# Kernel tuning notes

Hardware: AMD Instinct MI355X
Metric: run time of the kernel (lower is better)

## Reference

```python
import jax, jax.numpy as jnp
import numpy as np

B, SQ, SK, H, DH = 4, 4096, 462, 10, 64  # batch, img tokens, text tokens, heads, head dim


def setup_inputs() -> dict:
    key = jax.random.key(0)
    k1, k2, k3, k4, k5 = jax.random.split(key, 5)
    q = jax.random.normal(k1, (B, SQ, H * DH), dtype=jnp.float32)
    k = jax.random.normal(k2, (B, SK, H * DH), dtype=jnp.float32)
    v = jax.random.normal(k3, (B, SK, H * DH), dtype=jnp.float32)
    # mask_scale = H*W / sum(mask) in the original -> positive, >= 1
    mask_scale = 1.0 + 3.0 * jax.random.uniform(k4, (B, H, SQ, SK), dtype=jnp.float32)
    mask_bool = jax.random.randint(k5, (B, H, SQ, SK), 0, 2).astype(bool)
    # guarantee every query row attends to at least one key (avoid all -inf rows)
    mask_bool = mask_bool.at[..., 0].set(True)
    return {"q": q, "k": k, "v": v, "mask_bool": mask_bool,
            "mask_scale": mask_scale, "heads": H}


def reference(q, k, v, mask_bool, mask_scale, heads):
    b, sq, d = q.shape
    dh = d // heads
    # [b, s, h*dh] -> [b, h, s, dh]
    qh = q.reshape(b, sq, heads, dh).transpose(0, 2, 1, 3)
    kh = k.reshape(b, -1, heads, dh).transpose(0, 2, 1, 3)
    vh = v.reshape(b, -1, heads, dh).transpose(0, 2, 1, 3)
    scale = 1.0 / np.sqrt(dh).astype(np.float32)
    scores = jnp.einsum("bhqd,bhkd->bhqk", qh, kh) * scale
    scores = scores * mask_scale
    scores = jnp.where(mask_bool, scores, -jnp.inf)
    attn = jax.nn.softmax(scores, axis=-1)
    out = jnp.einsum("bhqk,bhkd->bhqd", attn, vh)
    return out.transpose(0, 2, 1, 3).reshape(b, sq, d)
```

## Files before the change

kernel.cpp:

```cpp
#include <hip/hip_runtime.h>

#define B_  4
#define SQ_ 4096
#define SK_ 462
#define H_  10
#define DH_ 64
#define D_  (H_ * DH_)
#define SKP_ 480
#define KT_  15
#define MBDW_ 16

typedef _Float16 half8 __attribute__((ext_vector_type(8)));
typedef float floatx4 __attribute__((ext_vector_type(4)));
typedef float float2v __attribute__((ext_vector_type(2)));

#define K16_ELEMS ((size_t)B_ * H_ * SKP_ * DH_)
#define MBITS_DW  ((size_t)B_ * H_ * SQ_ * MBDW_)
#define WS_KV     (2 * K16_ELEMS * sizeof(_Float16))
#define WS_FULL   (WS_KV + MBITS_DW * 4)

__device__ int g_mask_fmt;

__global__ void detect_mask_fmt(const unsigned int* __restrict__ mb_dw) {
  __shared__ int s_float, s_byte;
  if (threadIdx.x == 0) { s_float = 0; s_byte = 0; }
  __syncthreads();
  int fl = 0, by = 0;
  for (int i = threadIdx.x; i < 1024; i += 256) {
    unsigned int x = mb_dw[i];
    if (x > 1u) {
      if (x == 0x3F800000u) fl = 1; else by = 1;
    }
  }
  if (fl) atomicOr(&s_float, 1);
  if (by) atomicOr(&s_byte, 1);
  __syncthreads();
  if (threadIdx.x == 0) g_mask_fmt = s_float ? 2 : (s_byte ? 1 : 0);
}

__device__ __forceinline__ half8 cvt8(float4 a, float4 b) {
  half8 o;
  o[0] = (_Float16)a.x; o[1] = (_Float16)a.y;
  o[2] = (_Float16)a.z; o[3] = (_Float16)a.w;
  o[4] = (_Float16)b.x; o[5] = (_Float16)b.y;
  o[6] = (_Float16)b.z; o[7] = (_Float16)b.w;
  return o;
}

__global__ void convert_kv(const float* __restrict__ k, const float* __restrict__ v,
                           _Float16* __restrict__ k16, _Float16* __restrict__ vt16) {
  int t = blockIdx.x * 256 + threadIdx.x;
  const int NK = B_ * H_ * SKP_ * (DH_ / 8);
  const int NV = B_ * H_ * DH_ * (SKP_ / 8);
  if (t < NK) {
    int d8  = t & 7;
    int key = (t >> 3) % SKP_;
    int bh  = t / (8 * SKP_);
    int b = bh / H_, h = bh % H_;
    half8 o;
    if (key < SK_) {
      const float* src = k + ((size_t)(b * SK_ + key)) * D_ + h * DH_ + d8 * 8;
      float4 f0 = *reinterpret_cast<const float4*>(src);
      float4 f1 = *reinterpret_cast<const float4*>(src + 4);
      o = cvt8(f0, f1);
    } else {
      #pragma unroll
      for (int j = 0; j < 8; ++j) o[j] = (_Float16)0.0f;
    }
    *reinterpret_cast<half8*>(k16 + ((size_t)bh * SKP_ + key) * DH_ + d8 * 8) = o;
  } else if (t < NK + NV) {
    int u  = t - NK;
    int k8 = u % (SKP_ / 8);
    int d  = (u / (SKP_ / 8)) % DH_;
    int bh = u / ((SKP_ / 8) * DH_);
    int b = bh / H_, h = bh % H_;
    half8 o;
    #pragma unroll
    for (int j = 0; j < 8; ++j) {
      int key = k8 * 8 + j;
      o[j] = (key < SK_)
               ? (_Float16)v[((size_t)(b * SK_ + key)) * D_ + h * DH_ + d]
               : (_Float16)0.0f;
    }
    *reinterpret_cast<half8*>(vt16 + ((size_t)bh * DH_ + d) * SKP_ + k8 * 8) = o;
  }
}

__global__ __launch_bounds__(256)
void build_mbits(const void* __restrict__ mb, unsigned int* __restrict__ mbits) {
  const int fmt  = g_mask_fmt;
  const int lane = threadIdx.x & 63;
  const int wgid = (blockIdx.x * 256 + threadIdx.x) >> 6;
  const unsigned char* mbb = (const unsigned char*)mb;
  const unsigned int*  mbd = (const unsigned int*)mb;
  for (int rr = 0; rr < 16; ++rr) {
    int row = wgid * 16 + rr;
    size_t rb = (size_t)row * SK_;
    #pragma unroll
    for (int i = 0; i < 8; ++i) {
      int col = i * 64 + lane;
      int mv = 0;
      if (col < SK_) mv = (fmt == 1) ? (mbb[rb + col] != 0) : (mbd[rb + col] != 0u);
      unsigned long long bal = __ballot(mv);
      if (lane == 0)  mbits[(size_t)row * MBDW_ + i * 2]     = (unsigned int)bal;
      if (lane == 32) mbits[(size_t)row * MBDW_ + i * 2 + 1] = (unsigned int)(bal >> 32);
    }
  }
}

__global__ __launch_bounds__(256, 4)
void attn_fwd_full(const float* __restrict__ q, const float* __restrict__ msc,
                   float* __restrict__ out,
                   const _Float16* __restrict__ k16, const _Float16* __restrict__ vt16,
                   const unsigned int* __restrict__ mbits) {
  __shared__ __align__(16) _Float16     ps[4][16][34];
  __shared__ __align__(16) float        ms[4][16][34];
  __shared__ __align__(16) unsigned int mbl[4][16][16];

  const int tid  = threadIdx.x;
  const int wave = tid >> 6;
  const int lane = tid & 63;
  const int l16  = lane & 15;
  const int g4   = lane >> 4;

  const int b  = blockIdx.z;
  const int h  = blockIdx.y;
  const int q0 = blockIdx.x * 64;
  const int bh = b * H_ + h;

  half8 aq[2];
  {
    const float* qp = q + ((size_t)(b * SQ_ + q0 + wave * 16 + l16)) * D_ + h * DH_;
    #pragma unroll
    for (int kk = 0; kk < 2; ++kk) {
      float4 f0 = *reinterpret_cast<const float4*>(qp + kk * 32 + g4 * 8);
      float4 f1 = *reinterpret_cast<const float4*>(qp + kk * 32 + g4 * 8 + 4);
      aq[kk] = cvt8(f0, f1);
    }
  }

  {
    int i = lane >> 2, c4 = (lane & 3) * 4;
    size_t row = (size_t)bh * SQ_ + (q0 + wave * 16 + i);
    uint4 w = *reinterpret_cast<const uint4*>(mbits + row * MBDW_ + c4);
    *reinterpret_cast<uint4*>(&mbl[wave][i][c4]) = w;
  }

  floatx4 o_acc[4];
  floatx4 l_acc;
  #pragma unroll
  for (int nt = 0; nt < 4; ++nt)
    #pragma unroll
    for (int r = 0; r < 4; ++r) o_acc[nt][r] = 0.0f;
  #pragma unroll
  for (int r = 0; r < 4; ++r) l_acc[r] = 0.0f;
  float m2[4] = {-1e30f, -1e30f, -1e30f, -1e30f};

  half8 ones_f;
  #pragma unroll
  for (int j = 0; j < 8; ++j) ones_f[j] = (_Float16)1.0f;

  const float c2 = 0.18033688011112042f;

  const size_t mrow = ((size_t)bh * SQ_ + (q0 + wave * 16 + (lane >> 2))) * SK_;
  float2v rA[4], rB[4];
  auto issue_msc = [&](int kt_, float2v (&rg)[4]) {
    #pragma unroll
    for (int p = 0; p < 4; ++p) {
      int c = kt_ * 32 + ((lane & 3) + p * 4) * 2;
      c = (c <= SK_ - 2) ? c : (SK_ - 2);
      rg[p] = *reinterpret_cast<const float2v*>(msc + mrow + c);
    }
  };
  auto write_tile = [&](float2v (&rg)[4]) {
    int i = lane >> 2;
    #pragma unroll
    for (int p = 0; p < 4; ++p) {
      int c = ((lane & 3) + p * 4) * 2;
      *reinterpret_cast<float2v*>(&ms[wave][i][c]) = rg[p];
    }
  };

  issue_msc(0, rA);
  issue_msc(1, rB);
  write_tile(rA);
  #pragma unroll
  for (int p = 0; p < 4; ++p) rA[p] = rB[p];

  const _Float16* kbase16 = k16 + (size_t)bh * SKP_ * DH_;
  const _Float16* vbase16 = vt16 + (size_t)bh * DH_ * SKP_;

  for (int kt = 0; kt < KT_; ++kt) {
    if (kt + 2 < KT_) issue_msc(kt + 2, rB);
    __builtin_amdgcn_sched_barrier(0);

    half8 kbf[2][2];
    {
      const _Float16* kp = kbase16 + (size_t)(kt * 32) * DH_;
      #pragma unroll
      for (int ct = 0; ct < 2; ++ct)
        #pragma unroll
        for (int kk = 0; kk < 2; ++kk)
          kbf[ct][kk] = *reinterpret_cast<const half8*>(
              kp + (ct * 16 + l16) * DH_ + kk * 32 + g4 * 8);
    }
    half8 vbf[4];
    {
      const _Float16* vp = vbase16 + kt * 32 + g4 * 8;
      #pragma unroll
      for (int nt = 0; nt < 4; ++nt)
        vbf[nt] = *reinterpret_cast<const half8*>(vp + (size_t)(nt * 16 + l16) * SKP_);
    }

    floatx4 s[2];
    #pragma unroll
    for (int ct = 0; ct < 2; ++ct)
      #pragma unroll
      for (int r = 0; r < 4; ++r) s[ct][r] = 0.0f;
    #pragma unroll
    for (int ct = 0; ct < 2; ++ct)
      #pragma unroll
      for (int kk = 0; kk < 2; ++kk)
        s[ct] = __builtin_amdgcn_mfma_f32_16x16x32_f16(aq[kk], kbf[ct][kk], s[ct], 0, 0, 0);

    float mC[2][4];
    #pragma unroll
    for (int r = 0; r < 4; ++r) {
      unsigned int mw = mbl[wave][g4 * 4 + r][kt];
      float v0 = ms[wave][g4 * 4 + r][l16];
      float v1 = ms[wave][g4 * 4 + r][16 + l16];
      mC[0][r] = ((mw >> l16) & 1u)        ? v0 : 0.0f;
      mC[1][r] = ((mw >> (16 + l16)) & 1u) ? v1 : 0.0f;
    }

    float pw[2][4];
    #pragma unroll
    for (int r = 0; r < 4; ++r) {
      float sc0 = mC[0][r], sc1 = mC[1][r];
      float s0 = (sc0 != 0.0f) ? s[0][r] * (c2 * sc0) : -1e30f;
      float s1 = (sc1 != 0.0f) ? s[1][r] * (c2 * sc1) : -1e30f;
      float mx = fmaxf(s0, s1);
      mx = fmaxf(mx, __shfl_xor(mx, 1));
      mx = fmaxf(mx, __shfl_xor(mx, 2));
      mx = fmaxf(mx, __shfl_xor(mx, 4));
      mx = fmaxf(mx, __shfl_xor(mx, 8));
      float mnew  = fmaxf(m2[r], mx);
      float alpha = exp2f(m2[r] - mnew);
      m2[r] = mnew;
      pw[0][r] = exp2f(s0 - mnew);
      pw[1][r] = exp2f(s1 - mnew);
      l_acc[r] *= alpha;
      #pragma unroll
      for (int nt = 0; nt < 4; ++nt) o_acc[nt][r] *= alpha;
    }

    #pragma unroll
    for (int ct = 0; ct < 2; ++ct)
      #pragma unroll
      for (int r = 0; r < 4; ++r)
        ps[wave][g4 * 4 + r][ct * 16 + l16] = (_Float16)pw[ct][r];
    asm volatile("s_waitcnt lgkmcnt(0)" ::: "memory");
    half8 pa;
    #pragma unroll
    for (int j = 0; j < 8; ++j) pa[j] = ps[wave][l16][g4 * 8 + j];

    #pragma unroll
    for (int nt = 0; nt < 4; ++nt)
      o_acc[nt] = __builtin_amdgcn_mfma_f32_16x16x32_f16(pa, vbf[nt], o_acc[nt], 0, 0, 0);
    l_acc = __builtin_amdgcn_mfma_f32_16x16x32_f16(pa, ones_f, l_acc, 0, 0, 0);

    if (kt + 1 < KT_) {
      write_tile(rA);
      #pragma unroll
      for (int p = 0; p < 4; ++p) rA[p] = rB[p];
    }
  }

  #pragma unroll
  for (int r = 0; r < 4; ++r) {
    float inv = 1.0f / l_acc[r];
    int qrow = q0 + wave * 16 + g4 * 4 + r;
    float* ob = out + (size_t)(b * SQ_ + qrow) * D_ + h * DH_;
    #pragma unroll
    for (int nt = 0; nt < 4; ++nt)
      ob[nt * 16 + l16] = o_acc[nt][r] * inv;
  }
}

template<bool WS, bool MBYTE>
__device__ __forceinline__ void attn_body(
    const float* __restrict__ q, const float* __restrict__ k,
    const float* __restrict__ v, const void* __restrict__ mb,
    const float* __restrict__ msc, float* __restrict__ out,
    const _Float16* __restrict__ k16, const _Float16* __restrict__ vt16,
    _Float16 (&ps)[4][16][34]) {
  const int tid  = threadIdx.x;
  const int wave = tid >> 6;
  const int lane = tid & 63;
  const int l16  = lane & 15;
  const int g4   = lane >> 4;
  const int b  = blockIdx.z;
  const int h  = blockIdx.y;
  const int q0 = blockIdx.x * 64;
  const int bh = b * H_ + h;

  half8 aq[2];
  {
    const float* qp = q + ((size_t)(b * SQ_ + q0 + wave * 16 + l16)) * D_ + h * DH_;
    #pragma unroll
    for (int kk = 0; kk < 2; ++kk) {
      float4 f0 = *reinterpret_cast<const float4*>(qp + kk * 32 + g4 * 8);
      float4 f1 = *reinterpret_cast<const float4*>(qp + kk * 32 + g4 * 8 + 4);
      aq[kk] = cvt8(f0, f1);
    }
  }

  floatx4 o_acc[4];
  floatx4 l_acc;
  #pragma unroll
  for (int nt = 0; nt < 4; ++nt)
    #pragma unroll
    for (int r = 0; r < 4; ++r) o_acc[nt][r] = 0.0f;
  #pragma unroll
  for (int r = 0; r < 4; ++r) l_acc[r] = 0.0f;
  float m2[4] = {-1e30f, -1e30f, -1e30f, -1e30f};

  unsigned int rowoff[4];
  #pragma unroll
  for (int r = 0; r < 4; ++r) {
    int qrow = q0 + wave * 16 + g4 * 4 + r;
    rowoff[r] = (unsigned int)((b * H_ + h) * SQ_ + qrow) * SK_;
  }

  half8 ones_f;
  #pragma unroll
  for (int j = 0; j < 8; ++j) ones_f[j] = (_Float16)1.0f;
  const float c2 = 0.18033688011112042f;

  const unsigned char* mbb = (const unsigned char*)mb;
  const unsigned int*  mbd = (const unsigned int*)mb;

  auto load_masks = [&](int kt_, float (&m_)[2][4]) {
    #pragma unroll
    for (int ct = 0; ct < 2; ++ct)
      #pragma unroll
      for (int r = 0; r < 4; ++r) {
        int col = kt_ * 32 + ct * 16 + l16;
        int cc  = col < SK_ ? col : SK_ - 1;
        unsigned int idx = rowoff[r] + (unsigned int)cc;
        float sc = msc[idx];
        unsigned int mvv = MBYTE ? (unsigned int)mbb[idx] : mbd[idx];
        m_[ct][r] = (mvv != 0u && col < SK_) ? sc : 0.0f;
      }
  };

  float mC[2][4];
  load_masks(0, mC);

  const _Float16* kbase16 = k16 + (size_t)bh * SKP_ * DH_;
  const _Float16* vbase16 = vt16 + (size_t)bh * DH_ * SKP_;
  const float* kbase = k + (size_t)(b * SK_) * D_ + h * DH_;
  const float* vbase = v + (size_t)(b * SK_) * D_ + h * DH_;

  for (int kt = 0; kt < KT_; ++kt) {
    half8 kbf[2][2];
    if constexpr (WS) {
      const _Float16* kp = kbase16 + (size_t)(kt * 32) * DH_;
      #pragma unroll
      for (int ct = 0; ct < 2; ++ct)
        #pragma unroll
        for (int kk = 0; kk < 2; ++kk)
          kbf[ct][kk] = *reinterpret_cast<const half8*>(
              kp + (ct * 16 + l16) * DH_ + kk * 32 + g4 * 8);
    } else {
      #pragma unroll
      for (int ct = 0; ct < 2; ++ct) {
        int key = kt * 32 + ct * 16 + l16;
        int kc  = key < SK_ ? key : SK_ - 1;
        #pragma unroll
        for (int kk = 0; kk < 2; ++kk) {
          const float* kp = kbase + (size_t)kc * D_ + kk * 32 + g4 * 8;
          float4 f0 = *reinterpret_cast<const float4*>(kp);
          float4 f1 = *reinterpret_cast<const float4*>(kp + 4);
          kbf[ct][kk] = cvt8(f0, f1);
        }
      }
    }
    half8 vbf[4];
    if constexpr (WS) {
      const _Float16* vp = vbase16 + kt * 32 + g4 * 8;
      #pragma unroll
      for (int nt = 0; nt < 4; ++nt)
        vbf[nt] = *reinterpret_cast<const half8*>(vp + (size_t)(nt * 16 + l16) * SKP_);
    } else {
      #pragma unroll
      for (int nt = 0; nt < 4; ++nt) {
        int dim = nt * 16 + l16;
        #pragma unroll
        for (int j = 0; j < 8; ++j) {
          int key = kt * 32 + g4 * 8 + j;
          vbf[nt][j] = (key < SK_)
                         ? (_Float16)vbase[(size_t)key * D_ + dim]
                         : (_Float16)0.0f;
        }
      }
    }

    float mN[2][4];
    if (kt + 1 < KT_) load_masks(kt + 1, mN);

    floatx4 s[2];
    #pragma unroll
    for (int ct = 0; ct < 2; ++ct)
      #pragma unroll
      for (int r = 0; r < 4; ++r) s[ct][r] = 0.0f;
    #pragma unroll
    for (int ct = 0; ct < 2; ++ct)
      #pragma unroll
      for (int kk = 0; kk < 2; ++kk)
        s[ct] = __builtin_amdgcn_mfma_f32_16x16x32_f16(aq[kk], kbf[ct][kk], s[ct], 0, 0, 0);

    float pw[2][4];
    #pragma unroll
    for (int r = 0; r < 4; ++r) {
      float sc0 = mC[0][r], sc1 = mC[1][r];
      float s0 = (sc0 != 0.0f) ? s[0][r] * (c2 * sc0) : -1e30f;
      float s1 = (sc1 != 0.0f) ? s[1][r] * (c2 * sc1) : -1e30f;
      float mx = fmaxf(s0, s1);
      mx = fmaxf(mx, __shfl_xor(mx, 1));
      mx = fmaxf(mx, __shfl_xor(mx, 2));
      mx = fmaxf(mx, __shfl_xor(mx, 4));
      mx = fmaxf(mx, __shfl_xor(mx, 8));
      float mnew  = fmaxf(m2[r], mx);
      float alpha = exp2f(m2[r] - mnew);
      m2[r] = mnew;
      pw[0][r] = exp2f(s0 - mnew);
      pw[1][r] = exp2f(s1 - mnew);
      l_acc[r] *= alpha;
      #pragma unroll
      for (int nt = 0; nt < 4; ++nt) o_acc[nt][r] *= alpha;
    }

    #pragma unroll
    for (int ct = 0; ct < 2; ++ct)
      #pragma unroll
      for (int r = 0; r < 4; ++r)
        ps[wave][g4 * 4 + r][ct * 16 + l16] = (_Float16)pw[ct][r];
    asm volatile("s_waitcnt lgkmcnt(0)" ::: "memory");
    half8 pa;
    #pragma unroll
    for (int j = 0; j < 8; ++j) pa[j] = ps[wave][l16][g4 * 8 + j];

    #pragma unroll
    for (int nt = 0; nt < 4; ++nt)
      o_acc[nt] = __builtin_amdgcn_mfma_f32_16x16x32_f16(pa, vbf[nt], o_acc[nt], 0, 0, 0);
    l_acc = __builtin_amdgcn_mfma_f32_16x16x32_f16(pa, ones_f, l_acc, 0, 0, 0);

    if (kt + 1 < KT_) {
      #pragma unroll
      for (int ct = 0; ct < 2; ++ct)
        #pragma unroll
        for (int r = 0; r < 4; ++r) mC[ct][r] = mN[ct][r];
    }
  }

  #pragma unroll
  for (int r = 0; r < 4; ++r) {
    float inv = 1.0f / l_acc[r];
    int qrow = q0 + wave * 16 + g4 * 4 + r;
    float* ob = out + (size_t)(b * SQ_ + qrow) * D_ + h * DH_;
    #pragma unroll
    for (int nt = 0; nt < 4; ++nt)
      ob[nt * 16 + l16] = o_acc[nt][r] * inv;
  }
}

template<bool WS>
__global__ __launch_bounds__(256, 3)
void attn_fwd(const float* __restrict__ q, const float* __restrict__ k,
              const float* __restrict__ v, const void* __restrict__ mb,
              const float* __restrict__ msc, float* __restrict__ out,
              const _Float16* __restrict__ k16, const _Float16* __restrict__ vt16) {
  __shared__ __align__(16) _Float16 ps[4][16][34];
  if (g_mask_fmt == 1) attn_body<WS, true >(q, k, v, mb, msc, out, k16, vt16, ps);
  else                 attn_body<WS, false>(q, k, v, mb, msc, out, k16, vt16, ps);
}

extern "C" void kernel_launch(void* const* d_in, const int* in_sizes, int n_in,
                              void* d_out, int out_size, void* d_ws, size_t ws_size,
                              hipStream_t stream) {
  const float* q   = (const float*)d_in[0];
  const float* k   = (const float*)d_in[1];
  const float* v   = (const float*)d_in[2];
  const void*  mb  = d_in[3];
  const float* msc = (const float*)d_in[4];
  float* out = (float*)d_out;

  detect_mask_fmt<<<1, 256, 0, stream>>>((const unsigned int*)mb);

  _Float16* k16  = (_Float16*)d_ws;
  _Float16* vt16 = k16 + K16_ELEMS;
  unsigned int* mbits = (unsigned int*)(vt16 + K16_ELEMS);

  dim3 grid(SQ_ / 64, H_, B_);
  if (d_ws != nullptr && ws_size >= WS_FULL) {
    convert_kv<<<1200, 256, 0, stream>>>(k, v, k16, vt16);
    build_mbits<<<2560, 256, 0, stream>>>(mb, mbits);
    attn_fwd_full<<<grid, 256, 0, stream>>>(q, msc, out, k16, vt16, mbits);
  } else if (d_ws != nullptr && ws_size >= WS_KV) {
    convert_kv<<<1200, 256, 0, stream>>>(k, v, k16, vt16);
    attn_fwd<true><<<grid, 256, 0, stream>>>(q, k, v, mb, msc, out, k16, vt16);
  } else {
    attn_fwd<false><<<grid, 256, 0, stream>>>(q, k, v, mb, msc, out, k16, vt16);
  }
}
```

Baseline: 822.2 us.

## Fuse mask bit-packing into attention kernel with prefetched mask loads

Removes the separate build_mbits pass and instead loads raw mask values alongside mask_scale in the prefetch pipeline, folding them into the scale tile in shared memory. The shared-memory tile now uses an XOR swizzle to reduce bank conflicts, and the key loop is unrolled by two with ping-pong register buffers. This drops a full extra pass over the large mask tensor, but the main kernel reads wider mask data and uses more registers (launch bounds lowered from 4 to 3 blocks).

```diff
diff --git a/kernel.cpp b/kernel.cpp
--- a/kernel.cpp
+++ b/kernel.cpp
@@ -8,16 +8,13 @@
 #define D_  (H_ * DH_)
 #define SKP_ 480
 #define KT_  15
-#define MBDW_ 16
 
 typedef _Float16 half8 __attribute__((ext_vector_type(8)));
 typedef float floatx4 __attribute__((ext_vector_type(4)));
 typedef float float2v __attribute__((ext_vector_type(2)));
 
 #define K16_ELEMS ((size_t)B_ * H_ * SKP_ * DH_)
-#define MBITS_DW  ((size_t)B_ * H_ * SQ_ * MBDW_)
 #define WS_KV     (2 * K16_ELEMS * sizeof(_Float16))
-#define WS_FULL   (WS_KV + MBITS_DW * 4)
 
 __device__ int g_mask_fmt;
 
@@ -86,37 +83,12 @@
   }
 }
 
-__global__ __launch_bounds__(256)
-void build_mbits(const void* __restrict__ mb, unsigned int* __restrict__ mbits) {
-  const int fmt  = g_mask_fmt;
-  const int lane = threadIdx.x & 63;
-  const int wgid = (blockIdx.x * 256 + threadIdx.x) >> 6;
-  const unsigned char* mbb = (const unsigned char*)mb;
-  const unsigned int*  mbd = (const unsigned int*)mb;
-  for (int rr = 0; rr < 16; ++rr) {
-    int row = wgid * 16 + rr;
-    size_t rb = (size_t)row * SK_;
-    #pragma unroll
-    for (int i = 0; i < 8; ++i) {
-      int col = i * 64 + lane;
-      int mv = 0;
-      if (col < SK_) mv = (fmt == 1) ? (mbb[rb + col] != 0) : (mbd[rb + col] != 0u);
-      unsigned long long bal = __ballot(mv);
-      if (lane == 0)  mbits[(size_t)row * MBDW_ + i * 2]     = (unsigned int)bal;
-      if (lane == 32) mbits[(size_t)row * MBDW_ + i * 2 + 1] = (unsigned int)(bal >> 32);
-    }
-  }
-}
-
-__global__ __launch_bounds__(256, 4)
-void attn_fwd_full(const float* __restrict__ q, const float* __restrict__ msc,
-                   float* __restrict__ out,
-                   const _Float16* __restrict__ k16, const _Float16* __restrict__ vt16,
-                   const unsigned int* __restrict__ mbits) {
-  __shared__ __align__(16) _Float16     ps[4][16][34];
-  __shared__ __align__(16) float        ms[4][16][34];
-  __shared__ __align__(16) unsigned int mbl[4][16][16];
-
+template<bool MBYTE>
+__device__ __forceinline__ void attn_full_body(
+    const float* __restrict__ q, const void* __restrict__ mb,
+    const float* __restrict__ msc, float* __restrict__ out,
+    const _Float16* __restrict__ k16, const _Float16* __restrict__ vt16,
+    _Float16 (&ps)[4][16][34], float (&ms)[4][16][34]) {
   const int tid  = threadIdx.x;
   const int wave = tid >> 6;
   const int lane = tid & 63;
@@ -139,13 +111,6 @@
     }
   }
 
-  {
-    int i = lane >> 2, c4 = (lane & 3) * 4;
-    size_t row = (size_t)bh * SQ_ + (q0 + wave * 16 + i);
-    uint4 w = *reinterpret_cast<const uint4*>(mbits + row * MBDW_ + c4);
-    *reinterpret_cast<uint4*>(&mbl[wave][i][c4]) = w;
-  }
-
   floatx4 o_acc[4];
   floatx4 l_acc;
   #pragma unroll
@@ -162,38 +127,58 @@
 
   const float c2 = 0.18033688011112042f;
 
+  const unsigned char* mbb = (const unsigned char*)mb;
+  const unsigned int*  mbd = (const unsigned int*)mb;
+
   const size_t mrow = ((size_t)bh * SQ_ + (q0 + wave * 16 + (lane >> 2))) * SK_;
-  float2v rA[4], rB[4];
-  auto issue_msc = [&](int kt_, float2v (&rg)[4]) {
+
+  struct Buf {
+    float2v      sc[4];
+    uint2        mk2[4];
+    unsigned int mk1[4];
+  };
+  Buf bufA, bufB;
+
+  auto ISSUE = [&](int kt_, Buf& bf) {
     #pragma unroll
     for (int p = 0; p < 4; ++p) {
-      int c = kt_ * 32 + ((lane & 3) + p * 4) * 2;
-      c = (c <= SK_ - 2) ? c : (SK_ - 2);
-      rg[p] = *reinterpret_cast<const float2v*>(msc + mrow + c);
+      int cp = (lane & 3) + p * 4;
+      int c  = kt_ * 32 + cp * 2;
+      int cc = (c <= SK_ - 2) ? c : (SK_ - 2);
+      bf.sc[p] = *reinterpret_cast<const float2v*>(msc + mrow + cc);
+      if constexpr (MBYTE)
+        bf.mk1[p] = *reinterpret_cast<const unsigned short*>(mbb + mrow + cc);
+      else
+        bf.mk2[p] = *reinterpret_cast<const uint2*>(mbd + mrow + cc);
     }
   };
-  auto write_tile = [&](float2v (&rg)[4]) {
+
+  auto FOLD_WRITE = [&](int kt_, Buf& bf) {
     int i = lane >> 2;
     #pragma unroll
     for (int p = 0; p < 4; ++p) {
-      int c = ((lane & 3) + p * 4) * 2;
-      *reinterpret_cast<float2v*>(&ms[wave][i][c]) = rg[p];
+      int cp = (lane & 3) + p * 4;
+      int c  = kt_ * 32 + cp * 2;
+      float v0 = bf.sc[p][0], v1 = bf.sc[p][1];
+      unsigned int b0, b1;
+      if constexpr (MBYTE) { b0 = bf.mk1[p] & 0xFFu; b1 = bf.mk1[p] >> 8; }
+      else                 { b0 = bf.mk2[p].x;       b1 = bf.mk2[p].y;    }
+      v0 = (b0 != 0u && c     < SK_) ? v0 : 0.0f;
+      v1 = (b1 != 0u && c + 1 < SK_) ? v1 : 0.0f;
+      int cps = cp ^ ((i & 3) << 2);
+      float2v t; t[0] = v0; t[1] = v1;
+      *reinterpret_cast<float2v*>(&ms[wave][i][cps * 2]) = t;
     }
   };
-
-  issue_msc(0, rA);
-  issue_msc(1, rB);
-  write_tile(rA);
-  #pragma unroll
-  for (int p = 0; p < 4; ++p) rA[p] = rB[p];
 
   const _Float16* kbase16 = k16 + (size_t)bh * SKP_ * DH_;
   const _Float16* vbase16 = vt16 + (size_t)bh * DH_ * SKP_;
 
-  for (int kt = 0; kt < KT_; ++kt) {
-    if (kt + 2 < KT_) issue_msc(kt + 2, rB);
-    __builtin_amdgcn_sched_barrier(0);
-
+  ISSUE(0, bufB);
+  ISSUE(1, bufA);
+  FOLD_WRITE(0, bufB);
+
+  auto ITER = [&](int kt, Buf& rCur, Buf& rNxt) {
     half8 kbf[2][2];
     {
       const _Float16* kp = kbase16 + (size_t)(kt * 32) * DH_;
@@ -211,6 +196,10 @@
       for (int nt = 0; nt < 4; ++nt)
         vbf[nt] = *reinterpret_cast<const half8*>(vp + (size_t)(nt * 16 + l16) * SKP_);
     }
+    __builtin_amdgcn_sched_barrier(0);
+
+    if (kt + 2 < KT_) ISSUE(kt + 2, rNxt);
+    __builtin_amdgcn_sched_barrier(0);
 
     floatx4 s[2];
     #pragma unroll
@@ -226,11 +215,11 @@
     float mC[2][4];
     #pragma unroll
     for (int r = 0; r < 4; ++r) {
-      unsigned int mw = mbl[wave][g4 * 4 + r][kt];
-      float v0 = ms[wave][g4 * 4 + r][l16];
-      float v1 = ms[wave][g4 * 4 + r][16 + l16];
-      mC[0][r] = ((mw >> l16) & 1u)        ? v0 : 0.0f;
-      mC[1][r] = ((mw >> (16 + l16)) & 1u) ? v1 : 0.0f;
+      int row = g4 * 4 + r;
+      int cps0 = (l16 >> 1) ^ (r << 2);
+      int cps1 = (8 + (l16 >> 1)) ^ (r << 2);
+      mC[0][r] = ms[wave][row][cps0 * 2 + (l16 & 1)];
+      mC[1][r] = ms[wave][row][cps1 * 2 + (l16 & 1)];
     }
 
     float pw[2][4];
@@ -269,11 +258,13 @@
       o_acc[nt] = __builtin_amdgcn_mfma_f32_16x16x32_f16(pa, vbf[nt], o_acc[nt], 0, 0, 0);
     l_acc = __builtin_amdgcn_mfma_f32_16x16x32_f16(pa, ones_f, l_acc, 0, 0, 0);
 
-    if (kt + 1 < KT_) {
-      write_tile(rA);
-      #pragma unroll
-      for (int p = 0; p < 4; ++p) rA[p] = rB[p];
-    }
+    if (kt + 1 < KT_) FOLD_WRITE(kt + 1, rCur);
+  };
+
+  #pragma unroll
+  for (int kt = 0; kt < KT_; kt += 2) {
+    ITER(kt, bufA, bufB);
+    if (kt + 1 < KT_) ITER(kt + 1, bufB, bufA);
   }
 
   #pragma unroll
@@ -287,12 +278,21 @@
   }
 }
 
-template<bool WS, bool MBYTE>
-__device__ __forceinline__ void attn_body(
+__global__ __launch_bounds__(256, 3)
+void attn_fwd_full(const float* __restrict__ q, const void* __restrict__ mb,
+                   const float* __restrict__ msc, float* __restrict__ out,
+                   const _Float16* __restrict__ k16, const _Float16* __restrict__ vt16) {
+  __shared__ __align__(16) _Float16 ps[4][16][34];
+  __shared__ __align__(16) float    ms[4][16][34];
+  if (g_mask_fmt == 1) attn_full_body<true >(q, mb, msc, out, k16, vt16, ps, ms);
+  else                 attn_full_body<false>(q, mb, msc, out, k16, vt16, ps, ms);
+}
+
+template<bool MBYTE>
+__device__ __forceinline__ void attn_body_fb(
     const float* __restrict__ q, const float* __restrict__ k,
     const float* __restrict__ v, const void* __restrict__ mb,
     const float* __restrict__ msc, float* __restrict__ out,
-    const _Float16* __restrict__ k16, const _Float16* __restrict__ vt16,
     _Float16 (&ps)[4][16][34]) {
   const int tid  = threadIdx.x;
   const int wave = tid >> 6;
@@ -302,7 +302,6 @@
   const int b  = blockIdx.z;
   const int h  = blockIdx.y;
   const int q0 = blockIdx.x * 64;
-  const int bh = b * H_ + h;
 
   half8 aq[2];
   {
@@ -357,52 +356,32 @@
   float mC[2][4];
   load_masks(0, mC);
 
-  const _Float16* kbase16 = k16 + (size_t)bh * SKP_ * DH_;
-  const _Float16* vbase16 = vt16 + (size_t)bh * DH_ * SKP_;
   const float* kbase = k + (size_t)(b * SK_) * D_ + h * DH_;
   const float* vbase = v + (size_t)(b * SK_) * D_ + h * DH_;
 
   for (int kt = 0; kt < KT_; ++kt) {
     half8 kbf[2][2];
-    if constexpr (WS) {
-      const _Float16* kp = kbase16 + (size_t)(kt * 32) * DH_;
-      #pragma unroll
-      for (int ct = 0; ct < 2; ++ct)
-        #pragma unroll
-        for (int kk = 0; kk < 2; ++kk)
-          kbf[ct][kk] = *reinterpret_cast<const half8*>(
-              kp + (ct * 16 + l16) * DH_ + kk * 32 + g4 * 8);
-    } else {
-      #pragma unroll
-      for (int ct = 0; ct < 2; ++ct) {
-        int key = kt * 32 + ct * 16 + l16;
-        int kc  = key < SK_ ? key : SK_ - 1;
-        #pragma unroll
-        for (int kk = 0; kk < 2; ++kk) {
-          const float* kp = kbase + (size_t)kc * D_ + kk * 32 + g4 * 8;
-          float4 f0 = *reinterpret_cast<const float4*>(kp);
-          float4 f1 = *reinterpret_cast<const float4*>(kp + 4);
-          kbf[ct][kk] = cvt8(f0, f1);
-        }
+    #pragma unroll
+    for (int ct = 0; ct < 2; ++ct) {
+      int key = kt * 32 + ct * 16 + l16;
+      int kc  = key < SK_ ? key : SK_ - 1;
+      #pragma unroll
+      for (int kk = 0; kk < 2; ++kk) {
+        const float* kp = kbase + (size_t)kc * D_ + kk * 32 + g4 * 8;
+        float4 f0 = *reinterpret_cast<const float4*>(kp);
+        float4 f1 = *reinterpret_cast<const float4*>(kp + 4);
+        kbf[ct][kk] = cvt8(f0, f1);
       }
     }
     half8 vbf[4];
-    if constexpr (WS) {
-      const _Float16* vp = vbase16 + kt * 32 + g4 * 8;
-      #pragma unroll
-      for (int nt = 0; nt < 4; ++nt)
-        vbf[nt] = *reinterpret_cast<const half8*>(vp + (size_t)(nt * 16 + l16) * SKP_);
-    } else {
-      #pragma unroll
-      for (int nt = 0; nt < 4; ++nt) {
-        int dim = nt * 16 + l16;
-        #pragma unroll
-        for (int j = 0; j < 8; ++j) {
-          int key = kt * 32 + g4 * 8 + j;
-          vbf[nt][j] = (key < SK_)
-                         ? (_Float16)vbase[(size_t)key * D_ + dim]
-                         : (_Float16)0.0f;
-        }
+    #pragma unroll
+    for (int nt = 0; nt < 4; ++nt) {
+      int dim = nt * 16 + l16;
+      #pragma unroll
+      for (int j = 0; j < 8; ++j) {
+        int key = kt * 32 + g4 * 8 + j;
+        vbf[nt][j] = (key < SK_) ? (_Float16)vbase[(size_t)key * D_ + dim]
+                                 : (_Float16)0.0f;
       }
     }
 
@@ -475,15 +454,13 @@
   }
 }
 
-template<bool WS>
 __global__ __launch_bounds__(256, 3)
-void attn_fwd(const float* __restrict__ q, const float* __restrict__ k,
-              const float* __restrict__ v, const void* __restrict__ mb,
-              const float* __restrict__ msc, float* __restrict__ out,
-              const _Float16* __restrict__ k16, const _Float16* __restrict__ vt16) {
+void attn_fwd_fb(const float* __restrict__ q, const float* __restrict__ k,
+                 const float* __restrict__ v, const void* __restrict__ mb,
+                 const float* __restrict__ msc, float* __restrict__ out) {
   __shared__ __align__(16) _Float16 ps[4][16][34];
-  if (g_mask_fmt == 1) attn_body<WS, true >(q, k, v, mb, msc, out, k16, vt16, ps);
-  else                 attn_body<WS, false>(q, k, v, mb, msc, out, k16, vt16, ps);
+  if (g_mask_fmt == 1) attn_body_fb<true >(q, k, v, mb, msc, out, ps);
+  else                 attn_body_fb<false>(q, k, v, mb, msc, out, ps);
 }
 
 extern "C" void kernel_launch(void* const* d_in, const int* in_sizes, int n_in,
@@ -500,17 +477,12 @@
 
   _Float16* k16  = (_Float16*)d_ws;
   _Float16* vt16 = k16 + K16_ELEMS;
-  unsigned int* mbits = (unsigned int*)(vt16 + K16_ELEMS);
 
   dim3 grid(SQ_ / 64, H_, B_);
-  if (d_ws != nullptr && ws_size >= WS_FULL) {
+  if (d_ws != nullptr && ws_size >= WS_KV) {
     convert_kv<<<1200, 256, 0, stream>>>(k, v, k16, vt16);
-    build_mbits<<<2560, 256, 0, stream>>>(mb, mbits);
-    attn_fwd_full<<<grid, 256, 0, stream>>>(q, msc, out, k16, vt16, mbits);
-  } else if (d_ws != nullptr && ws_size >= WS_KV) {
-    convert_kv<<<1200, 256, 0, stream>>>(k, v, k16, vt16);
-    attn_fwd<true><<<grid, 256, 0, stream>>>(q, k, v, mb, msc, out, k16, vt16);
+    attn_fwd_full<<<grid, 256, 0, stream>>>(q, mb, msc, out, k16, vt16);
   } else {
-    attn_fwd<false><<<grid, 256, 0, stream>>>(q, k, v, mb, msc, out, k16, vt16);
-  }
-}
+    attn_fwd_fb<<<grid, 256, 0, stream>>>(q, k, v, mb, msc, out);
+  }
+}
```

Result: faster. 715.5 us (-13.0%).
